# Kernel tuning notes

Hardware: AMD Instinct MI355X
Metric: run time of the kernel (lower is better)

The kernel has to match this reference:

```python
import jax, jax.numpy as jnp
import numpy as np

B, N, T, P, H = 256, 101, 128, 4, 16


def _conv2d(x, w, dil=(1, 1), pad=((0, 0), (0, 0))):
    # x: [B,C,H,W] NCHW, w: [O,I,kh,kw] OIHW
    return jax.lax.conv_general_dilated(
        x, w, window_strides=(1, 1), padding=pad, rhs_dilation=dil,
        dimension_numbers=('NCHW', 'OIHW', 'NCHW'))


def _tccb(x, d1, d2, cc, r, dil, pad):
    # residual branch: 1x1 conv only when channels change (r is None otherwise)
    res = _conv2d(x, r) if r is not None else x
    h = jnp.pad(x, ((0, 0), (0, 0), (0, 0), (pad, 0)))  # causal left-pad on time
    h = jax.nn.relu(_conv2d(h, d1, dil=(1, dil)))
    h = jnp.pad(h, ((0, 0), (0, 0), (0, 0), (pad, 0)))
    h = jax.nn.relu(_conv2d(h, d2, dil=(1, dil)))
    h = jax.nn.relu(_conv2d(h, cc, pad=((5, 5), (0, 0))))  # cross-stock (11,1) conv
    return jax.nn.relu(res + h)


def setup_inputs() -> dict:
    key = jax.random.key(0)
    ks = jax.random.split(key, 21)
    s = 0.05
    rn = lambda k, shape: jax.random.normal(k, shape, jnp.float32) * s
    return {
        'x': jax.random.normal(ks[0], (B, N, T, P), jnp.float32),
        'proj_w': rn(ks[1], (P, P)), 'proj_b': rn(ks[2], (P,)),
        'w_ih': rn(ks[3], (4 * H, P)), 'w_hh': rn(ks[4], (4 * H, H)),
        'b_ih': rn(ks[5], (4 * H,)), 'b_hh': rn(ks[6], (4 * H,)),
        't1_d1': rn(ks[7], (8, 4, 1, 3)), 't1_d2': rn(ks[8], (8, 8, 1, 3)),
        't1_c': rn(ks[9], (8, 8, 11, 1)), 't1_r': rn(ks[10], (8, 4, 1, 1)),
        't2_d1': rn(ks[11], (16, 8, 1, 3)), 't2_d2': rn(ks[12], (16, 16, 1, 3)),
        't2_c': rn(ks[13], (16, 16, 11, 1)), 't2_r': rn(ks[14], (16, 8, 1, 1)),
        't3_d1': rn(ks[15], (16, 16, 1, 3)), 't3_d2': rn(ks[16], (16, 16, 1, 3)),
        't3_c': rn(ks[17], (16, 16, 11, 1)),
        'conv4_w': rn(ks[18], (16, 16, 1, T)),
        'out_w': rn(ks[19], (1, 2 * H)), 'out_b': rn(ks[20], (1,)),
    }


def reference(x, proj_w, proj_b, w_ih, w_hh, b_ih, b_hh,
              t1_d1, t1_d2, t1_c, t1_r,
              t2_d1, t2_d2, t2_c, t2_r,
              t3_d1, t3_d2, t3_c,
              conv4_w, out_w, out_b):
    b, n = x.shape[0], x.shape[1]
    # linear_proj over the feature dim P (eval mode: dropout off)
    x_proj_f = x @ proj_w.T + proj_b          # [B,N,T,P]
    x_proj = jnp.transpose(x_proj_f, (0, 3, 1, 2))  # [B,P,N,T]

    # LSTM: torch runs one nn.LSTM call per stock with shared weights ->
    # exactly equivalent to vectorizing the stock dim alongside batch.
    xs = jnp.transpose(x_proj_f, (2, 0, 1, 3))  # [T,B,N,P]

    def step(carry, xt):
        h, c = carry
        g = xt @ w_ih.T + b_ih + h @ w_hh.T + b_hh  # [B,N,4H], gate order i,f,g,o
        i, f, gg, o = jnp.split(g, 4, axis=-1)
        c = jax.nn.sigmoid(f) * c + jax.nn.sigmoid(i) * jnp.tanh(gg)
        h = jax.nn.sigmoid(o) * jnp.tanh(c)
        return (h, c), None

    h0 = jnp.zeros((b, n, H), x.dtype)
    (h_last, _), _ = jax.lax.scan(step, (h0, h0), xs)  # h_last: [B,N,H]
    # faithful to torch: result is [N,B,H] then .view(B,N,H) (a reshape, not transpose)
    x_lstm = jnp.transpose(h_last, (1, 0, 2)).reshape(b, n, H)
    x_lstm = jnp.transpose(x_lstm, (0, 2, 1))  # [B,H,N]

    h1 = _tccb(x_proj, t1_d1, t1_d2, t1_c, t1_r, 1, 2)
    h2 = _tccb(h1, t2_d1, t2_d2, t2_c, t2_r, 2, 4)
    h3 = _tccb(h2, t3_d1, t3_d2, t3_c, None, 4, 8)
    h4 = jax.nn.relu(_conv2d(h3, conv4_w))[..., 0]  # [B,16,N]

    out = jnp.concatenate([x_lstm, h4], axis=1)      # [B,32,N]
    out = jnp.transpose(out, (0, 2, 1)) @ out_w.T + out_b  # [B,N,1]
    return jax.nn.softmax(out[..., 0], axis=-1)      # [B,N]
```

## Files before the change

kernel.cpp:

```cpp
#include <hip/hip_runtime.h>
#include <hip/hip_bf16.h>

constexpr int B = 256;
constexpr int N = 101;
constexpr int T = 128;

typedef float vf2 __attribute__((ext_vector_type(2)));
typedef short s8v __attribute__((ext_vector_type(8)));
typedef unsigned short u8v __attribute__((ext_vector_type(8)));
typedef unsigned short u4s __attribute__((ext_vector_type(4)));
typedef float f4v __attribute__((ext_vector_type(4)));

__device__ __forceinline__ float frcp(float x) { return __builtin_amdgcn_rcpf(x); }
__device__ __forceinline__ float sigmoidf_(float x) { return frcp(1.f + __expf(-x)); }
__device__ __forceinline__ float tanhf_(float x) { return 2.f * frcp(1.f + __expf(-2.f * x)) - 1.f; }

__device__ __forceinline__ unsigned short f2bf(float x) {
  unsigned int u = __float_as_uint(x);
  u = (u + 0x7FFFu + ((u >> 16) & 1u)) >> 16;
  return (unsigned short)u;
}
__device__ __forceinline__ float bf2f(unsigned short u) {
  return __uint_as_float((unsigned int)u << 16);
}

__device__ __forceinline__ int swz_n(int L) {
  int q = L & 7, r = L >> 3;
  return q * 13 - (q > 5 ? (q - 5) : 0) + r;
}

__global__ __launch_bounds__(64) void lstm_kernel(
    const float* __restrict__ x, const float* __restrict__ pw,
    const float* __restrict__ pb, const float* __restrict__ w_ih,
    const float* __restrict__ w_hh, const float* __restrict__ b_ih,
    const float* __restrict__ b_hh, float* __restrict__ h_out) {
  __shared__ vf2 sh[4][16];
  const int lane = threadIdx.x;
  const int sub = lane >> 4;
  const int k = lane & 15;
  const int row = blockIdx.x * 8 + sub * 2;

  float wf[4][4], whh[4][16], bias[4];
#pragma unroll
  for (int q = 0; q < 4; q++) {
    const int j = q * 16 + k;
    float bp = b_ih[j] + b_hh[j];
#pragma unroll
    for (int c = 0; c < 4; c++) bp += w_ih[j * 4 + c] * pb[c];
    bias[q] = bp;
#pragma unroll
    for (int p = 0; p < 4; p++) {
      float s = 0.f;
#pragma unroll
      for (int c = 0; c < 4; c++) s += w_ih[j * 4 + c] * pw[c * 4 + p];
      wf[q][p] = s;
    }
#pragma unroll
    for (int m = 0; m < 16; m++) whh[q][m] = w_hh[j * 16 + m];
  }

  vf2 h = {0.f, 0.f}, c = {0.f, 0.f};
  sh[sub][k] = h;
  const float4* xpA = (const float4*)x + (size_t)row * T;
  const float4* xpB = xpA + T;

#pragma unroll 1
  for (int t = 0; t < T; t++) {
    __syncthreads();
    float4 xa = xpA[t];
    float4 xb = xpB[t];
    vf2 xc0 = {xa.x, xb.x}, xc1 = {xa.y, xb.y};
    vf2 xc2 = {xa.z, xb.z}, xc3 = {xa.w, xb.w};
    vf2 a0 = {bias[0], bias[0]}, a1 = {bias[1], bias[1]};
    vf2 a2 = {bias[2], bias[2]}, a3 = {bias[3], bias[3]};
    a0 += wf[0][0] * xc0 + wf[0][1] * xc1 + wf[0][2] * xc2 + wf[0][3] * xc3;
    a1 += wf[1][0] * xc0 + wf[1][1] * xc1 + wf[1][2] * xc2 + wf[1][3] * xc3;
    a2 += wf[2][0] * xc0 + wf[2][1] * xc1 + wf[2][2] * xc2 + wf[2][3] * xc3;
    a3 += wf[3][0] * xc0 + wf[3][1] * xc1 + wf[3][2] * xc2 + wf[3][3] * xc3;
#pragma unroll
    for (int mm = 0; mm < 4; mm++) {
      vf2 hm0 = sh[sub][mm * 4 + 0];
      vf2 hm1 = sh[sub][mm * 4 + 1];
      vf2 hm2 = sh[sub][mm * 4 + 2];
      vf2 hm3 = sh[sub][mm * 4 + 3];
      a0 += whh[0][mm * 4 + 0] * hm0 + whh[0][mm * 4 + 1] * hm1 +
            whh[0][mm * 4 + 2] * hm2 + whh[0][mm * 4 + 3] * hm3;
      a1 += whh[1][mm * 4 + 0] * hm0 + whh[1][mm * 4 + 1] * hm1 +
            whh[1][mm * 4 + 2] * hm2 + whh[1][mm * 4 + 3] * hm3;
      a2 += whh[2][mm * 4 + 0] * hm0 + whh[2][mm * 4 + 1] * hm1 +
            whh[2][mm * 4 + 2] * hm2 + whh[2][mm * 4 + 3] * hm3;
      a3 += whh[3][mm * 4 + 0] * hm0 + whh[3][mm * 4 + 1] * hm1 +
            whh[3][mm * 4 + 2] * hm2 + whh[3][mm * 4 + 3] * hm3;
    }
    vf2 ig, fg, gg, og, tc;
    ig.x = sigmoidf_(a0.x); ig.y = sigmoidf_(a0.y);
    fg.x = sigmoidf_(a1.x); fg.y = sigmoidf_(a1.y);
    gg.x = tanhf_(a2.x);    gg.y = tanhf_(a2.y);
    og.x = sigmoidf_(a3.x); og.y = sigmoidf_(a3.y);
    c = fg * c + ig * gg;
    tc.x = tanhf_(c.x);     tc.y = tanhf_(c.y);
    h = og * tc;
    __syncthreads();
    sh[sub][k] = h;
  }
  h_out[(size_t)row * 16 + k] = h.x;
  h_out[(size_t)(row + 1) * 16 + k] = h.y;
}

__global__ void prep_kernel(const float* __restrict__ t1c,
                            const float* __restrict__ t2c,
                            const float* __restrict__ t3c,
                            const float* __restrict__ t2d1,
                            const float* __restrict__ t2d2,
                            const float* __restrict__ t3d1,
                            const float* __restrict__ t3d2,
                            unsigned short* __restrict__ apk) {
  const int L = threadIdx.x;
  const int co = L & 15, q = L >> 4;
#pragma unroll 1
  for (int set = 0; set < 15; set++) {
    int s, p;
    if (set < 3) { s = 0; p = set; }
    else if (set < 9) { s = 1; p = set - 3; }
    else { s = 2; p = set - 9; }
    u8v f;
#pragma unroll
    for (int j = 0; j < 8; j++) {
      float val = 0.f;
      if (s == 0) {
        int dn = p * 4 + q, ci = j;
        if (co < 8 && dn < 11) val = t1c[(co * 8 + ci) * 11 + dn];
      } else {
        int dn = p * 2 + (q >> 1), ci = (q & 1) * 8 + j;
        const float* w = (s == 1) ? t2c : t3c;
        if (dn < 11) val = w[(co * 16 + ci) * 11 + dn];
      }
      f[j] = f2bf(val);
    }
    *(u8v*)&apk[(set * 64 + L) * 8] = f;
  }
#pragma unroll 1
  for (int ds = 0; ds < 7; ds++) {
    const float* w; int CIw, CIeff, kk;
    switch (ds) {
      case 0: w = t2d1; CIw = 8;  CIeff = 8;  kk = 0; break;
      case 1: w = t2d2; CIw = 16; CIeff = 16; kk = 0; break;
      case 2: w = t2d2; CIw = 16; CIeff = 16; kk = 1; break;
      case 3: w = t3d1; CIw = 16; CIeff = 16; kk = 0; break;
      case 4: w = t3d1; CIw = 16; CIeff = 16; kk = 1; break;
      case 5: w = t3d2; CIw = 16; CIeff = 16; kk = 0; break;
      default: w = t3d2; CIw = 16; CIeff = 16; kk = 1; break;
    }
    u8v f;
#pragma unroll
    for (int j = 0; j < 8; j++) {
      int kg = kk * 32 + q * 8 + j;
      int ci = kg % CIeff, jt = kg / CIeff;
      float val = (jt < 3) ? w[(co * CIw + ci) * 3 + jt] : 0.f;
      f[j] = f2bf(val);
    }
    *(u8v*)&apk[((15 + ds) * 64 + L) * 8] = f;
  }
}

__global__ __launch_bounds__(128) void d12a_kernel(
    const float* __restrict__ xin,
    const float* __restrict__ pw, const float* __restrict__ pb,
    const float* __restrict__ w1,
    const float* __restrict__ w2,
    unsigned short* __restrict__ out, int b0) {
  constexpr int CI = 4, CO = 8, DIL = 1;
  const int t = threadIdx.x;
  const int n = swz_n(blockIdx.x), by = blockIdx.y;
  const int b = b0 + by;

  float r1[3][CO];
#pragma unroll
  for (int u = 0; u < 3; u++)
#pragma unroll
    for (int co = 0; co < CO; co++) r1[u][co] = 0.f;

  const float4* xp = (const float4*)xin + ((size_t)b * N + n) * T;
  float px[5][4];
#pragma unroll
  for (int v = 0; v < 5; v++) {
    int idx = t - v * DIL;
    float4 xr = xp[idx < 0 ? 0 : idx];
    bool ok = idx >= 0;
    px[v][0] = ok ? pb[0] + pw[0] * xr.x + pw[1] * xr.y + pw[2] * xr.z + pw[3] * xr.w : 0.f;
    px[v][1] = ok ? pb[1] + pw[4] * xr.x + pw[5] * xr.y + pw[6] * xr.z + pw[7] * xr.w : 0.f;
    px[v][2] = ok ? pb[2] + pw[8] * xr.x + pw[9] * xr.y + pw[10] * xr.z + pw[11] * xr.w : 0.f;
    px[v][3] = ok ? pb[3] + pw[12] * xr.x + pw[13] * xr.y + pw[14] * xr.z + pw[15] * xr.w : 0.f;
  }
#pragma unroll
  for (int ci = 0; ci < CI; ci++) {
#pragma unroll
    for (int j = 0; j < 3; j++) {
#pragma unroll
      for (int co = 0; co < CO; co++) {
        float w = w1[(co * CI + ci) * 3 + j];
#pragma unroll
        for (int u = 0; u < 3; u++) r1[u][co] += w * px[u + 2 - j][ci];
      }
    }
  }
#pragma unroll
  for (int u = 0; u < 3; u++)
#pragma unroll
    for (int co = 0; co < CO; co++) r1[u][co] = fmaxf(r1[u][co], 0.f);

  float acc[CO];
#pragma unroll
  for (int co = 0; co < CO; co++) acc[co] = 0.f;
#pragma unroll
  for (int cm = 0; cm < CO; cm++) {
#pragma unroll
    for (int j = 0; j < 3; j++) {
#pragma unroll
      for (int co = 0; co < CO; co++)
        acc[co] += w2[(co * CO + cm) * 3 + j] * r1[2 - j][cm];
    }
  }
  unsigned short* op = &out[(((size_t)by * N + n) * T + t) * CO];
  u8v a;
#pragma unroll
  for (int j = 0; j < 8; j++) a[j] = f2bf(fmaxf(acc[j], 0.f));
  *(u8v*)&op[0] = a;
}

template <int C, int DIL>
__global__ __launch_bounds__(64) void cd2_kernel(
    const unsigned short* __restrict__ zin,
    const unsigned short* __restrict__ apkc,
    const unsigned short* __restrict__ apkd,
    const void* __restrict__ resin,
    const float* __restrict__ rw,
    const float* __restrict__ pw, const float* __restrict__ pb,
    unsigned short* __restrict__ hout,
    unsigned short* __restrict__ zout,
    int b0) {
  constexpr int NMF = (C == 8) ? 3 : 6;
  constexpr int HALO = 8;
  __shared__ __align__(16) unsigned short Hs[HALO + T][C];
  __shared__ __align__(16) unsigned short Rs[HALO + T][16];
  const int l = threadIdx.x;
  const int tcol = l & 15, q = l >> 4;
  const int n = swz_n(blockIdx.x);
  const int by = blockIdx.y;
  const int b = b0 + by;

  if (l < 16) {
    *(u8v*)&Rs[l >> 1][(l & 1) * 8] = (u8v)0;
    if constexpr (C == 8) {
      if (l < 8) *(u8v*)&Hs[l][0] = (u8v)0;
    } else {
      *(u8v*)&Hs[l >> 1][(l & 1) * 8] = (u8v)0;
    }
  }

  s8v ac[NMF];
#pragma unroll
  for (int p = 0; p < NMF; p++) ac[p] = *(const s8v*)&apkc[(p * 64 + l) * 8];
  constexpr int ND1 = (C == 8) ? 1 : 2;
  s8v a1_0 = *(const s8v*)&apkd[(0 * 64 + l) * 8];
  s8v a1_1 = a1_0;
  if constexpr (C == 16) a1_1 = *(const s8v*)&apkd[(1 * 64 + l) * 8];
  s8v a2_0 = *(const s8v*)&apkd[((ND1 + 0) * 64 + l) * 8];
  s8v a2_1 = *(const s8v*)&apkd[((ND1 + 1) * 64 + l) * 8];

#pragma unroll 1
  for (int tt = 0; tt < 8; tt++) {
    const int t = tt * 16 + tcol;
    f4v d = (f4v)0.f;
#pragma unroll
    for (int p = 0; p < NMF; p++) {
      int dn = (C == 8) ? (p * 4 + q) : (p * 2 + (q >> 1));
      int row = n + dn - 5;
      bool ok = (unsigned)row < (unsigned)N;
      int rowc = ok ? row : 0;
      const unsigned short* bp =
          &zin[(((size_t)by * N + rowc) * T + t) * C + ((C == 16) ? (q & 1) * 8 : 0)];
      s8v bfrag = *(const s8v*)bp;
      if (!ok) bfrag = (s8v){0, 0, 0, 0, 0, 0, 0, 0};
      d = __builtin_amdgcn_mfma_f32_16x16x32_bf16(ac[p], bfrag, d, 0, 0, 0);
    }
    if constexpr (C == 8) {
      if (q < 2) {
        float4 xr = ((const float4*)resin)[((size_t)b * N + n) * T + t];
        float xv[4];
#pragma unroll
        for (int j = 0; j < 4; j++)
          xv[j] = pb[j] + pw[j * 4 + 0] * xr.x + pw[j * 4 + 1] * xr.y +
                  pw[j * 4 + 2] * xr.z + pw[j * 4 + 3] * xr.w;
        u4s hb16;
#pragma unroll
        for (int r = 0; r < 4; r++) {
          int co = q * 4 + r;
          float rv = rw[co * 4 + 0] * xv[0] + rw[co * 4 + 1] * xv[1] +
                     rw[co * 4 + 2] * xv[2] + rw[co * 4 + 3] * xv[3];
          hb16[r] = f2bf(fmaxf(rv + fmaxf(d[r], 0.f), 0.f));
        }
        *(u4s*)&hout[(((size_t)by * N + n) * T + t) * 8 + q * 4] = hb16;
        *(u4s*)&Hs[HALO + t][q * 4] = hb16;
      }
    } else {
      const unsigned short* hp =
          (const unsigned short*)resin + (((size_t)by * N + n) * T + t) * 8;
      u8v hb = *(const u8v*)hp;
      float hv[8];
#pragma unroll
      for (int ci = 0; ci < 8; ci++) hv[ci] = bf2f(hb[ci]);
      u4s hb16;
#pragma unroll
      for (int r = 0; r < 4; r++) {
        int co = q * 4 + r;
        float rv = 0.f;
#pragma unroll
        for (int ci = 0; ci < 8; ci++) rv += rw[co * 8 + ci] * hv[ci];
        hb16[r] = f2bf(fmaxf(rv + fmaxf(d[r], 0.f), 0.f));
      }
      *(u4s*)&hout[(((size_t)by * N + n) * T + t) * 16 + q * 4] = hb16;
      *(u4s*)&Hs[HALO + t][q * 4] = hb16;
    }
  }
  __syncthreads();

#pragma unroll 2
  for (int tt = 0; tt < 8; tt++) {
    const int t = tt * 16 + tcol;
    f4v acc = (f4v)0.f;
    if constexpr (C == 8) {
      const int jt = (q < 3) ? q : 2;
      s8v bf = *(const s8v*)&Hs[HALO + t - DIL * jt][0];
      acc = __builtin_amdgcn_mfma_f32_16x16x32_bf16(a1_0, bf, acc, 0, 0, 0);
    } else {
      {
        const int jt = q >> 1, ci0 = (q & 1) * 8;
        s8v bf = *(const s8v*)&Hs[HALO + t - DIL * jt][ci0];
        acc = __builtin_amdgcn_mfma_f32_16x16x32_bf16(a1_0, bf, acc, 0, 0, 0);
      }
      {
        const int ci0 = (q & 1) * 8;
        s8v bf = *(const s8v*)&Hs[HALO + t - DIL * 2][ci0];
        acc = __builtin_amdgcn_mfma_f32_16x16x32_bf16(a1_1, bf, acc, 0, 0, 0);
      }
    }
    u4s rb;
#pragma unroll
    for (int r = 0; r < 4; r++) rb[r] = f2bf(fmaxf(acc[r], 0.f));
    *(u4s*)&Rs[HALO + t][q * 4] = rb;
  }
  __syncthreads();

  unsigned short* opb = &zout[((size_t)by * N + n) * T * 16];
#pragma unroll 2
  for (int tt = 0; tt < 8; tt++) {
    const int t = tt * 16 + tcol;
    f4v acc = (f4v)0.f;
    {
      const int jt = q >> 1, ci0 = (q & 1) * 8;
      s8v bf = *(const s8v*)&Rs[HALO + t - DIL * jt][ci0];
      acc = __builtin_amdgcn_mfma_f32_16x16x32_bf16(a2_0, bf, acc, 0, 0, 0);
    }
    {
      const int ci0 = (q & 1) * 8;
      s8v bf = *(const s8v*)&Rs[HALO + t - DIL * 2][ci0];
      acc = __builtin_amdgcn_mfma_f32_16x16x32_bf16(a2_1, bf, acc, 0, 0, 0);
    }
    u4s ob;
#pragma unroll
    for (int r = 0; r < 4; r++) ob[r] = f2bf(fmaxf(acc[r], 0.f));
    *(u4s*)&opb[(size_t)t * 16 + q * 4] = ob;
  }
}

__global__ __launch_bounds__(64) void cy_kernel(
    const unsigned short* __restrict__ zin,
    const unsigned short* __restrict__ apkc,
    const unsigned short* __restrict__ resin,
    const float* __restrict__ w4,
    float* __restrict__ h4,
    int b0) {
  __shared__ __align__(16) float Ys[16][T + 2];
  const int l = threadIdx.x;
  const int tcol = l & 15, q = l >> 4;
  const int n = swz_n(blockIdx.x);
  const int by = blockIdx.y;
  const int b = b0 + by;

  s8v ac[6];
#pragma unroll
  for (int p = 0; p < 6; p++) ac[p] = *(const s8v*)&apkc[(p * 64 + l) * 8];

#pragma unroll 1
  for (int tt = 0; tt < 8; tt++) {
    const int t = tt * 16 + tcol;
    f4v d = (f4v)0.f;
#pragma unroll
    for (int p = 0; p < 6; p++) {
      int dn = p * 2 + (q >> 1);
      int row = n + dn - 5;
      bool ok = (unsigned)row < (unsigned)N;
      int rowc = ok ? row : 0;
      const unsigned short* bp =
          &zin[(((size_t)by * N + rowc) * T + t) * 16 + (q & 1) * 8];
      s8v bfrag = *(const s8v*)bp;
      if (!ok) bfrag = (s8v){0, 0, 0, 0, 0, 0, 0, 0};
      d = __builtin_amdgcn_mfma_f32_16x16x32_bf16(ac[p], bfrag, d, 0, 0, 0);
    }
    const unsigned short* hp = resin + (((size_t)by * N + n) * T + t) * 16 + q * 4;
    u4s hb = *(const u4s*)hp;
#pragma unroll
    for (int r = 0; r < 4; r++)
      Ys[q * 4 + r][t] = fmaxf(bf2f(hb[r]) + fmaxf(d[r], 0.f), 0.f);
  }
  __syncthreads();

  const int t0 = l * 2;
  vf2 y[16];
#pragma unroll
  for (int ci = 0; ci < 16; ci++) y[ci] = *(const vf2*)&Ys[ci][t0];

#pragma unroll 1
  for (int o = 0; o < 16; o++) {
    vf2 s = (vf2)0.f;
#pragma unroll
    for (int ci = 0; ci < 16; ci++) {
      vf2 w = *(const vf2*)&w4[(size_t)(o * 16 + ci) * T + t0];
      s += w * y[ci];
    }
    float sum = s.x + s.y;
    sum += __shfl_down(sum, 32);
    sum += __shfl_down(sum, 16);
    sum += __shfl_down(sum, 8);
    sum += __shfl_down(sum, 4);
    sum += __shfl_down(sum, 2);
    sum += __shfl_down(sum, 1);
    if (l == 0) h4[((size_t)b * 16 + o) * N + n] = fmaxf(sum, 0.f);
  }
}

__global__ __launch_bounds__(128) void final_kernel(
    const float* __restrict__ hl, const float* __restrict__ h4,
    const float* __restrict__ ow, const float* __restrict__ ob,
    float* __restrict__ out) {
  __shared__ float red[128];
  int b = blockIdx.x, n = threadIdx.x;
  bool valid = n < N;
  float lv = 0.f;
  if (valid) {
    int idx = b * N + n;
    int sb = idx & (B - 1);
    int sn = idx >> 8;
    const float* h = &hl[((size_t)sb * N + sn) * 16];
    float a = ob[0];
#pragma unroll
    for (int k = 0; k < 16; k++) a += h[k] * ow[k];
#pragma unroll
    for (int c = 0; c < 16; c++) a += h4[((size_t)b * 16 + c) * N + n] * ow[16 + c];
    lv = a;
  }
  red[n] = valid ? lv : -1e30f;
  __syncthreads();
  for (int off = 64; off > 0; off >>= 1) {
    if (n < off) red[n] = fmaxf(red[n], red[n + off]);
    __syncthreads();
  }
  float m = red[0];
  __syncthreads();
  float e = valid ? __expf(lv - m) : 0.f;
  red[n] = e;
  __syncthreads();
  for (int off = 64; off > 0; off >>= 1) {
    if (n < off) red[n] += red[n + off];
    __syncthreads();
  }
  float s = red[0];
  if (valid) out[(size_t)b * N + n] = e / s;
}

extern "C" void kernel_launch(void* const* d_in, const int* in_sizes, int n_in,
                              void* d_out, int out_size, void* d_ws, size_t ws_size,
                              hipStream_t stream) {
  const float* x    = (const float*)d_in[0];
  const float* pw   = (const float*)d_in[1];
  const float* pb   = (const float*)d_in[2];
  const float* w_ih = (const float*)d_in[3];
  const float* w_hh = (const float*)d_in[4];
  const float* b_ih = (const float*)d_in[5];
  const float* b_hh = (const float*)d_in[6];
  const float* t1d1 = (const float*)d_in[7];
  const float* t1d2 = (const float*)d_in[8];
  const float* t1c  = (const float*)d_in[9];
  const float* t1r  = (const float*)d_in[10];
  const float* t2d1 = (const float*)d_in[11];
  const float* t2d2 = (const float*)d_in[12];
  const float* t2c  = (const float*)d_in[13];
  const float* t2r  = (const float*)d_in[14];
  const float* t3d1 = (const float*)d_in[15];
  const float* t3d2 = (const float*)d_in[16];
  const float* t3c  = (const float*)d_in[17];
  const float* w4   = (const float*)d_in[18];
  const float* ow   = (const float*)d_in[19];
  const float* ob   = (const float*)d_in[20];
  float* outp = (float*)d_out;

  const size_t NT = (size_t)N * T;
  const size_t Bn16 = (size_t)B * N * 16;
  const size_t unit = 32 * NT;
  const size_t fixed = 2 * Bn16 + 8192;

  int Bc = 4;
  const int cands[7] = {256, 128, 64, 32, 16, 8, 4};
  for (int i = 0; i < 7; i++) {
    if ((cands[i] * unit + fixed) * sizeof(float) <= ws_size) { Bc = cands[i]; break; }
  }

  float* ws = (float*)d_ws;
  float* hl = ws;
  float* h4 = hl + Bn16;
  unsigned short* apk = (unsigned short*)(h4 + Bn16);
  float* p = h4 + Bn16 + 8192;
  unsigned short* Zb1  = (unsigned short*)p; p += (size_t)Bc * 4 * NT;
  unsigned short* H1b  = (unsigned short*)p; p += (size_t)Bc * 4 * NT;
  unsigned short* Zb2a = (unsigned short*)p; p += (size_t)Bc * 8 * NT;
  unsigned short* H2b  = (unsigned short*)p; p += (size_t)Bc * 8 * NT;
  unsigned short* Zb2b = (unsigned short*)p;

  prep_kernel<<<1, 64, 0, stream>>>(t1c, t2c, t3c, t2d1, t2d2, t3d1, t3d2, apk);
  lstm_kernel<<<(B * N) / 8, 64, 0, stream>>>(x, pw, pb, w_ih, w_hh, b_ih,
                                              b_hh, hl);

  dim3 g(N, Bc);
  for (int b0 = 0; b0 < B; b0 += Bc) {
    d12a_kernel<<<g, 128, 0, stream>>>(x, pw, pb, t1d1, t1d2, Zb1, b0);
    cd2_kernel<8, 2><<<g, 64, 0, stream>>>(
        Zb1, apk + 0 * 512, apk + 15 * 512, x, t1r, pw, pb, H1b, Zb2a, b0);
    cd2_kernel<16, 4><<<g, 64, 0, stream>>>(
        Zb2a, apk + 3 * 512, apk + 18 * 512, H1b, t2r, pw, pb, H2b, Zb2b, b0);
    cy_kernel<<<g, 64, 0, stream>>>(Zb2b, apk + 9 * 512, H2b, w4, h4, b0);
  }

  final_kernel<<<B, 128, 0, stream>>>(hl, h4, ow, ob, outp);
}
```

Baseline: 803.1 us.

## Use DPP row rotation for LSTM recurrence and split conv kernels across four waves

The LSTM hidden-state exchange now uses DPP row_ror:1 lane rotations within each 16-lane row instead of shared memory plus two barriers per timestep. The recurrent weights are pre-permuted to match the rotation direction, which is detected at runtime. Separately, the cd2 and cy conv kernels are launched with 256 threads, so each of the four waves handles two of the eight time tiles (and four output channels in cy) rather than one wave looping over all eight. This aims to cut LDS and barrier latency on the serial LSTM critical path and to raise per-block parallelism in the conv stages.

New measurement: 884.7 us. 1.1x slower.

```diff
diff --git a/kernel.cpp b/kernel.cpp
--- a/kernel.cpp
+++ b/kernel.cpp
@@ -29,18 +29,27 @@
   return q * 13 - (q > 5 ? (q - 5) : 0) + r;
 }
 
+__device__ __forceinline__ int rot1_i(int v) {
+  return __builtin_amdgcn_mov_dpp(v, 0x121, 0xf, 0xf, false);
+}
+__device__ __forceinline__ float rot1_f(float v) {
+  return __int_as_float(rot1_i(__float_as_int(v)));
+}
+
 __global__ __launch_bounds__(64) void lstm_kernel(
     const float* __restrict__ x, const float* __restrict__ pw,
     const float* __restrict__ pb, const float* __restrict__ w_ih,
     const float* __restrict__ w_hh, const float* __restrict__ b_ih,
     const float* __restrict__ b_hh, float* __restrict__ h_out) {
-  __shared__ vf2 sh[4][16];
   const int lane = threadIdx.x;
   const int sub = lane >> 4;
   const int k = lane & 15;
   const int row = blockIdx.x * 8 + sub * 2;
 
-  float wf[4][4], whh[4][16], bias[4];
+  const int rotm = rot1_i(lane);
+  const int step = (rotm == sub * 16 + ((k + 1) & 15)) ? 1 : 15;
+
+  float wf[4][4], wr[4][16], bias[4];
 #pragma unroll
   for (int q = 0; q < 4; q++) {
     const int j = q * 16 + k;
@@ -56,17 +65,16 @@
       wf[q][p] = s;
     }
 #pragma unroll
-    for (int m = 0; m < 16; m++) whh[q][m] = w_hh[j * 16 + m];
+    for (int i = 0; i < 16; i++)
+      wr[q][i] = w_hh[j * 16 + ((k + i * step) & 15)];
   }
 
   vf2 h = {0.f, 0.f}, c = {0.f, 0.f};
-  sh[sub][k] = h;
   const float4* xpA = (const float4*)x + (size_t)row * T;
   const float4* xpB = xpA + T;
 
 #pragma unroll 1
   for (int t = 0; t < T; t++) {
-    __syncthreads();
     float4 xa = xpA[t];
     float4 xb = xpB[t];
     vf2 xc0 = {xa.x, xb.x}, xc1 = {xa.y, xb.y};
@@ -78,19 +86,13 @@
     a2 += wf[2][0] * xc0 + wf[2][1] * xc1 + wf[2][2] * xc2 + wf[2][3] * xc3;
     a3 += wf[3][0] * xc0 + wf[3][1] * xc1 + wf[3][2] * xc2 + wf[3][3] * xc3;
 #pragma unroll
-    for (int mm = 0; mm < 4; mm++) {
-      vf2 hm0 = sh[sub][mm * 4 + 0];
-      vf2 hm1 = sh[sub][mm * 4 + 1];
-      vf2 hm2 = sh[sub][mm * 4 + 2];
-      vf2 hm3 = sh[sub][mm * 4 + 3];
-      a0 += whh[0][mm * 4 + 0] * hm0 + whh[0][mm * 4 + 1] * hm1 +
-            whh[0][mm * 4 + 2] * hm2 + whh[0][mm * 4 + 3] * hm3;
-      a1 += whh[1][mm * 4 + 0] * hm0 + whh[1][mm * 4 + 1] * hm1 +
-            whh[1][mm * 4 + 2] * hm2 + whh[1][mm * 4 + 3] * hm3;
-      a2 += whh[2][mm * 4 + 0] * hm0 + whh[2][mm * 4 + 1] * hm1 +
-            whh[2][mm * 4 + 2] * hm2 + whh[2][mm * 4 + 3] * hm3;
-      a3 += whh[3][mm * 4 + 0] * hm0 + whh[3][mm * 4 + 1] * hm1 +
-            whh[3][mm * 4 + 2] * hm2 + whh[3][mm * 4 + 3] * hm3;
+    for (int i = 0; i < 16; i++) {
+      a0 += wr[0][i] * h;
+      a1 += wr[1][i] * h;
+      a2 += wr[2][i] * h;
+      a3 += wr[3][i] * h;
+      h.x = rot1_f(h.x);
+      h.y = rot1_f(h.y);
     }
     vf2 ig, fg, gg, og, tc;
     ig.x = sigmoidf_(a0.x); ig.y = sigmoidf_(a0.y);
@@ -100,8 +102,6 @@
     c = fg * c + ig * gg;
     tc.x = tanhf_(c.x);     tc.y = tanhf_(c.y);
     h = og * tc;
-    __syncthreads();
-    sh[sub][k] = h;
   }
   h_out[(size_t)row * 16 + k] = h.x;
   h_out[(size_t)(row + 1) * 16 + k] = h.y;
@@ -229,7 +229,7 @@
 }
 
 template <int C, int DIL>
-__global__ __launch_bounds__(64) void cd2_kernel(
+__global__ __launch_bounds__(256) void cd2_kernel(
     const unsigned short* __restrict__ zin,
     const unsigned short* __restrict__ apkc,
     const unsigned short* __restrict__ apkd,
@@ -244,7 +244,9 @@
   __shared__ __align__(16) unsigned short Hs[HALO + T][C];
   __shared__ __align__(16) unsigned short Rs[HALO + T][16];
   const int l = threadIdx.x;
-  const int tcol = l & 15, q = l >> 4;
+  const int wv = l >> 6;
+  const int wl = l & 63;
+  const int tcol = wl & 15, q = wl >> 4;
   const int n = swz_n(blockIdx.x);
   const int by = blockIdx.y;
   const int b = b0 + by;
@@ -260,16 +262,17 @@
 
   s8v ac[NMF];
 #pragma unroll
-  for (int p = 0; p < NMF; p++) ac[p] = *(const s8v*)&apkc[(p * 64 + l) * 8];
+  for (int p = 0; p < NMF; p++) ac[p] = *(const s8v*)&apkc[(p * 64 + wl) * 8];
   constexpr int ND1 = (C == 8) ? 1 : 2;
-  s8v a1_0 = *(const s8v*)&apkd[(0 * 64 + l) * 8];
+  s8v a1_0 = *(const s8v*)&apkd[(0 * 64 + wl) * 8];
   s8v a1_1 = a1_0;
-  if constexpr (C == 16) a1_1 = *(const s8v*)&apkd[(1 * 64 + l) * 8];
-  s8v a2_0 = *(const s8v*)&apkd[((ND1 + 0) * 64 + l) * 8];
-  s8v a2_1 = *(const s8v*)&apkd[((ND1 + 1) * 64 + l) * 8];
-
-#pragma unroll 1
-  for (int tt = 0; tt < 8; tt++) {
+  if constexpr (C == 16) a1_1 = *(const s8v*)&apkd[(1 * 64 + wl) * 8];
+  s8v a2_0 = *(const s8v*)&apkd[((ND1 + 0) * 64 + wl) * 8];
+  s8v a2_1 = *(const s8v*)&apkd[((ND1 + 1) * 64 + wl) * 8];
+
+#pragma unroll
+  for (int s = 0; s < 2; s++) {
+    const int tt = wv * 2 + s;
     const int t = tt * 16 + tcol;
     f4v d = (f4v)0.f;
 #pragma unroll
@@ -325,8 +328,9 @@
   }
   __syncthreads();
 
-#pragma unroll 2
-  for (int tt = 0; tt < 8; tt++) {
+#pragma unroll
+  for (int s = 0; s < 2; s++) {
+    const int tt = wv * 2 + s;
     const int t = tt * 16 + tcol;
     f4v acc = (f4v)0.f;
     if constexpr (C == 8) {
@@ -353,8 +357,9 @@
   __syncthreads();
 
   unsigned short* opb = &zout[((size_t)by * N + n) * T * 16];
-#pragma unroll 2
-  for (int tt = 0; tt < 8; tt++) {
+#pragma unroll
+  for (int s = 0; s < 2; s++) {
+    const int tt = wv * 2 + s;
     const int t = tt * 16 + tcol;
     f4v acc = (f4v)0.f;
     {
@@ -374,7 +379,7 @@
   }
 }
 
-__global__ __launch_bounds__(64) void cy_kernel(
+__global__ __launch_bounds__(256) void cy_kernel(
     const unsigned short* __restrict__ zin,
     const unsigned short* __restrict__ apkc,
     const unsigned short* __restrict__ resin,
@@ -383,17 +388,20 @@
     int b0) {
   __shared__ __align__(16) float Ys[16][T + 2];
   const int l = threadIdx.x;
-  const int tcol = l & 15, q = l >> 4;
+  const int wv = l >> 6;
+  const int wl = l & 63;
+  const int tcol = wl & 15, q = wl >> 4;
   const int n = swz_n(blockIdx.x);
   const int by = blockIdx.y;
   const int b = b0 + by;
 
   s8v ac[6];
 #pragma unroll
-  for (int p = 0; p < 6; p++) ac[p] = *(const s8v*)&apkc[(p * 64 + l) * 8];
-
-#pragma unroll 1
-  for (int tt = 0; tt < 8; tt++) {
+  for (int p = 0; p < 6; p++) ac[p] = *(const s8v*)&apkc[(p * 64 + wl) * 8];
+
+#pragma unroll
+  for (int s = 0; s < 2; s++) {
+    const int tt = wv * 2 + s;
     const int t = tt * 16 + tcol;
     f4v d = (f4v)0.f;
 #pragma unroll
@@ -416,13 +424,14 @@
   }
   __syncthreads();
 
-  const int t0 = l * 2;
+  const int t0 = wl * 2;
   vf2 y[16];
 #pragma unroll
   for (int ci = 0; ci < 16; ci++) y[ci] = *(const vf2*)&Ys[ci][t0];
 
 #pragma unroll 1
-  for (int o = 0; o < 16; o++) {
+  for (int oo = 0; oo < 4; oo++) {
+    const int o = wv * 4 + oo;
     vf2 s = (vf2)0.f;
 #pragma unroll
     for (int ci = 0; ci < 16; ci++) {
@@ -436,7 +445,7 @@
     sum += __shfl_down(sum, 4);
     sum += __shfl_down(sum, 2);
     sum += __shfl_down(sum, 1);
-    if (l == 0) h4[((size_t)b * 16 + o) * N + n] = fmaxf(sum, 0.f);
+    if (wl == 0) h4[((size_t)b * 16 + o) * N + n] = fmaxf(sum, 0.f);
   }
 }
 
@@ -534,11 +543,11 @@
   dim3 g(N, Bc);
   for (int b0 = 0; b0 < B; b0 += Bc) {
     d12a_kernel<<<g, 128, 0, stream>>>(x, pw, pb, t1d1, t1d2, Zb1, b0);
-    cd2_kernel<8, 2><<<g, 64, 0, stream>>>(
+    cd2_kernel<8, 2><<<g, 256, 0, stream>>>(
         Zb1, apk + 0 * 512, apk + 15 * 512, x, t1r, pw, pb, H1b, Zb2a, b0);
-    cd2_kernel<16, 4><<<g, 64, 0, stream>>>(
+    cd2_kernel<16, 4><<<g, 256, 0, stream>>>(
         Zb2a, apk + 3 * 512, apk + 18 * 512, H1b, t2r, pw, pb, H2b, Zb2b, b0);
-    cy_kernel<<<g, 64, 0, stream>>>(Zb2b, apk + 9 * 512, H2b, w4, h4, b0);
+    cy_kernel<<<g, 256, 0, stream>>>(Zb2b, apk + 9 * 512, H2b, w4, h4, b0);
   }
 
   final_kernel<<<B, 128, 0, stream>>>(hl, h4, ow, ob, outp);
```

## Compute LSTM gate matmuls with bf16 MFMA and shuffle-based hidden-state exchange

Applied to the files above, without the earlier changes.

The LSTM kernel now computes the input and recurrent gate products for 16 sequences per wavefront with four 16x16x32 bf16 MFMA instructions per step. The weights are packed into A fragments once, and the hidden state is passed between lanes with shuffles instead of shared memory and barriers. The next timestep's input is prefetched during the current step. The recurrence is now done in bf16 precision, which may accumulate error over the 128 steps.

Measured after the change: 744.5 us. 1.08x faster.

```diff
diff --git a/kernel.cpp b/kernel.cpp
--- a/kernel.cpp
+++ b/kernel.cpp
@@ -9,6 +9,7 @@
 typedef short s8v __attribute__((ext_vector_type(8)));
 typedef unsigned short u8v __attribute__((ext_vector_type(8)));
 typedef unsigned short u4s __attribute__((ext_vector_type(4)));
+typedef unsigned int u32x4 __attribute__((ext_vector_type(4)));
 typedef float f4v __attribute__((ext_vector_type(4)));
 
 __device__ __forceinline__ float frcp(float x) { return __builtin_amdgcn_rcpf(x); }
@@ -22,6 +23,9 @@
 }
 __device__ __forceinline__ float bf2f(unsigned short u) {
   return __uint_as_float((unsigned int)u << 16);
+}
+__device__ __forceinline__ unsigned pack2(float a, float b) {
+  return (unsigned)f2bf(a) | ((unsigned)f2bf(b) << 16);
 }
 
 __device__ __forceinline__ int swz_n(int L) {
@@ -34,77 +38,89 @@
     const float* __restrict__ pb, const float* __restrict__ w_ih,
     const float* __restrict__ w_hh, const float* __restrict__ b_ih,
     const float* __restrict__ b_hh, float* __restrict__ h_out) {
-  __shared__ vf2 sh[4][16];
-  const int lane = threadIdx.x;
-  const int sub = lane >> 4;
-  const int k = lane & 15;
-  const int row = blockIdx.x * 8 + sub * 2;
-
-  float wf[4][4], whh[4][16], bias[4];
-#pragma unroll
-  for (int q = 0; q < 4; q++) {
-    const int j = q * 16 + k;
-    float bp = b_ih[j] + b_hh[j];
-#pragma unroll
-    for (int c = 0; c < 4; c++) bp += w_ih[j * 4 + c] * pb[c];
-    bias[q] = bp;
+  const int l = threadIdx.x;
+  const int s = l & 15;
+  const int q = l >> 4;
+  const int row0 = blockIdx.x * 16;
+
+  s8v Afr[4];
+#pragma unroll
+  for (int m = 0; m < 4; m++) {
+    const int j = m * 16 + s;
+    float wfm[4];
 #pragma unroll
     for (int p = 0; p < 4; p++) {
-      float s = 0.f;
-#pragma unroll
-      for (int c = 0; c < 4; c++) s += w_ih[j * 4 + c] * pw[c * 4 + p];
-      wf[q][p] = s;
-    }
-#pragma unroll
-    for (int m = 0; m < 16; m++) whh[q][m] = w_hh[j * 16 + m];
-  }
-
-  vf2 h = {0.f, 0.f}, c = {0.f, 0.f};
-  sh[sub][k] = h;
-  const float4* xpA = (const float4*)x + (size_t)row * T;
-  const float4* xpB = xpA + T;
+      float v = 0.f;
+#pragma unroll
+      for (int c = 0; c < 4; c++) v += w_ih[j * 4 + c] * pw[c * 4 + p];
+      wfm[p] = v;
+    }
+    u8v av;
+#pragma unroll
+    for (int j2 = 0; j2 < 8; j2++) {
+      const int k = q * 8 + j2;
+      float val = (k < 4) ? wfm[k] : ((k < 20) ? w_hh[j * 16 + (k - 4)] : 0.f);
+      av[j2] = f2bf(val);
+    }
+    Afr[m] = *(s8v*)&av;
+  }
+  float bi[4][4];
+#pragma unroll
+  for (int m = 0; m < 4; m++) {
+#pragma unroll
+    for (int r = 0; r < 4; r++) {
+      const int jb = m * 16 + q * 4 + r;
+      float bp = b_ih[jb] + b_hh[jb];
+#pragma unroll
+      for (int c = 0; c < 4; c++) bp += w_ih[jb * 4 + c] * pb[c];
+      bi[m][r] = bp;
+    }
+  }
+
+  const float4* xp = (const float4*)x + (size_t)(row0 + s) * T;
+  float4 xa = xp[0];
+  float c0 = 0.f, c1 = 0.f, c2 = 0.f, c3 = 0.f;
+  float h0 = 0.f, h1 = 0.f, h2 = 0.f, h3 = 0.f;
 
 #pragma unroll 1
   for (int t = 0; t < T; t++) {
-    __syncthreads();
-    float4 xa = xpA[t];
-    float4 xb = xpB[t];
-    vf2 xc0 = {xa.x, xb.x}, xc1 = {xa.y, xb.y};
-    vf2 xc2 = {xa.z, xb.z}, xc3 = {xa.w, xb.w};
-    vf2 a0 = {bias[0], bias[0]}, a1 = {bias[1], bias[1]};
-    vf2 a2 = {bias[2], bias[2]}, a3 = {bias[3], bias[3]};
-    a0 += wf[0][0] * xc0 + wf[0][1] * xc1 + wf[0][2] * xc2 + wf[0][3] * xc3;
-    a1 += wf[1][0] * xc0 + wf[1][1] * xc1 + wf[1][2] * xc2 + wf[1][3] * xc3;
-    a2 += wf[2][0] * xc0 + wf[2][1] * xc1 + wf[2][2] * xc2 + wf[2][3] * xc3;
-    a3 += wf[3][0] * xc0 + wf[3][1] * xc1 + wf[3][2] * xc2 + wf[3][3] * xc3;
-#pragma unroll
-    for (int mm = 0; mm < 4; mm++) {
-      vf2 hm0 = sh[sub][mm * 4 + 0];
-      vf2 hm1 = sh[sub][mm * 4 + 1];
-      vf2 hm2 = sh[sub][mm * 4 + 2];
-      vf2 hm3 = sh[sub][mm * 4 + 3];
-      a0 += whh[0][mm * 4 + 0] * hm0 + whh[0][mm * 4 + 1] * hm1 +
-            whh[0][mm * 4 + 2] * hm2 + whh[0][mm * 4 + 3] * hm3;
-      a1 += whh[1][mm * 4 + 0] * hm0 + whh[1][mm * 4 + 1] * hm1 +
-            whh[1][mm * 4 + 2] * hm2 + whh[1][mm * 4 + 3] * hm3;
-      a2 += whh[2][mm * 4 + 0] * hm0 + whh[2][mm * 4 + 1] * hm1 +
-            whh[2][mm * 4 + 2] * hm2 + whh[2][mm * 4 + 3] * hm3;
-      a3 += whh[3][mm * 4 + 0] * hm0 + whh[3][mm * 4 + 1] * hm1 +
-            whh[3][mm * 4 + 2] * hm2 + whh[3][mm * 4 + 3] * hm3;
-    }
-    vf2 ig, fg, gg, og, tc;
-    ig.x = sigmoidf_(a0.x); ig.y = sigmoidf_(a0.y);
-    fg.x = sigmoidf_(a1.x); fg.y = sigmoidf_(a1.y);
-    gg.x = tanhf_(a2.x);    gg.y = tanhf_(a2.y);
-    og.x = sigmoidf_(a3.x); og.y = sigmoidf_(a3.y);
-    c = fg * c + ig * gg;
-    tc.x = tanhf_(c.x);     tc.y = tanhf_(c.y);
-    h = og * tc;
-    __syncthreads();
-    sh[sub][k] = h;
-  }
-  h_out[(size_t)row * 16 + k] = h.x;
-  h_out[(size_t)(row + 1) * 16 + k] = h.y;
+    const int tn = (t + 1 < T) ? t + 1 : t;
+    float4 xn = xp[tn];
+
+    unsigned A0 = pack2(h0, h1), A1 = pack2(h2, h3);
+    unsigned U0 = __shfl(A0, (l + 16) & 63);
+    unsigned U1 = __shfl(A1, (l + 16) & 63);
+    unsigned X0 = pack2(xa.x, xa.y), X1 = pack2(xa.z, xa.w);
+    unsigned b0 = (q == 0) ? X0 : ((q == 1) ? A0 : ((q == 2) ? U0 : 0u));
+    unsigned b1 = (q == 0) ? X1 : ((q == 1) ? A1 : ((q == 2) ? U1 : 0u));
+    unsigned b2 = (q == 0) ? A0 : ((q == 1) ? U0 : 0u);
+    unsigned b3 = (q == 0) ? A1 : ((q == 1) ? U1 : 0u);
+    u32x4 bu = {b0, b1, b2, b3};
+    s8v Bfr = *(s8v*)&bu;
+
+    f4v d0 = __builtin_amdgcn_mfma_f32_16x16x32_bf16(Afr[0], Bfr, (f4v)0.f, 0, 0, 0);
+    f4v d1 = __builtin_amdgcn_mfma_f32_16x16x32_bf16(Afr[1], Bfr, (f4v)0.f, 0, 0, 0);
+    f4v d2 = __builtin_amdgcn_mfma_f32_16x16x32_bf16(Afr[2], Bfr, (f4v)0.f, 0, 0, 0);
+    f4v d3 = __builtin_amdgcn_mfma_f32_16x16x32_bf16(Afr[3], Bfr, (f4v)0.f, 0, 0, 0);
+
+    float iv, fv, gv, ov;
+    iv = sigmoidf_(d0[0] + bi[0][0]); fv = sigmoidf_(d1[0] + bi[1][0]);
+    gv = tanhf_(d2[0] + bi[2][0]);    ov = sigmoidf_(d3[0] + bi[3][0]);
+    c0 = fv * c0 + iv * gv;           h0 = ov * tanhf_(c0);
+    iv = sigmoidf_(d0[1] + bi[0][1]); fv = sigmoidf_(d1[1] + bi[1][1]);
+    gv = tanhf_(d2[1] + bi[2][1]);    ov = sigmoidf_(d3[1] + bi[3][1]);
+    c1 = fv * c1 + iv * gv;           h1 = ov * tanhf_(c1);
+    iv = sigmoidf_(d0[2] + bi[0][2]); fv = sigmoidf_(d1[2] + bi[1][2]);
+    gv = tanhf_(d2[2] + bi[2][2]);    ov = sigmoidf_(d3[2] + bi[3][2]);
+    c2 = fv * c2 + iv * gv;           h2 = ov * tanhf_(c2);
+    iv = sigmoidf_(d0[3] + bi[0][3]); fv = sigmoidf_(d1[3] + bi[1][3]);
+    gv = tanhf_(d2[3] + bi[2][3]);    ov = sigmoidf_(d3[3] + bi[3][3]);
+    c3 = fv * c3 + iv * gv;           h3 = ov * tanhf_(c3);
+
+    xa = xn;
+  }
+  float* op = &h_out[(size_t)(row0 + s) * 16 + q * 4];
+  op[0] = h0; op[1] = h1; op[2] = h2; op[3] = h3;
 }
 
 __global__ void prep_kernel(const float* __restrict__ t1c,
@@ -528,8 +544,8 @@
   unsigned short* Zb2b = (unsigned short*)p;
 
   prep_kernel<<<1, 64, 0, stream>>>(t1c, t2c, t3c, t2d1, t2d2, t3d1, t3d2, apk);
-  lstm_kernel<<<(B * N) / 8, 64, 0, stream>>>(x, pw, pb, w_ih, w_hh, b_ih,
-                                              b_hh, hl);
+  lstm_kernel<<<(B * N) / 16, 64, 0, stream>>>(x, pw, pb, w_ih, w_hh, b_ih,
+                                               b_hh, hl);
 
   dim3 g(N, Bc);
   for (int b0 = 0; b0 < B; b0 += Bc) {
```
